# Kernel tuning notes

Measured on AMD Instinct MI355X. Metric: run time of the kernel, lower is better.

Reference implementation:

```python
import jax, jax.numpy as jnp
import numpy as np

NUM_HEADS = 8
EPS = 1e-9


def setup_inputs() -> dict:
    key = jax.random.key(0)
    ks = jax.random.split(key, 5)
    B, S, D = 2, 2048, 512
    x = jax.random.normal(ks[0], (B, S, D), dtype=jnp.float32)
    Wq = jax.random.normal(ks[1], (D, D), dtype=jnp.float32) * (1.0 / np.sqrt(D))
    Wk = jax.random.normal(ks[2], (D, D), dtype=jnp.float32) * (1.0 / np.sqrt(D))
    Wv = jax.random.normal(ks[3], (D, D), dtype=jnp.float32) * (1.0 / np.sqrt(D))
    Wo = jax.random.normal(ks[4], (D, D), dtype=jnp.float32) * (1.0 / np.sqrt(D))
    gamma = jnp.ones((D,), dtype=jnp.float32)
    beta = jnp.zeros((D,), dtype=jnp.float32)
    return {"x": x, "Wq": Wq, "Wk": Wk, "Wv": Wv, "Wo": Wo, "gamma": gamma, "beta": beta}


def _layernorm(x, gamma, beta):
    mean = jnp.mean(x, axis=-1, keepdims=True)
    var = jnp.mean(jnp.square(x - mean), axis=-1, keepdims=True)
    return gamma * ((x - mean) * jax.lax.rsqrt(var + EPS)) + beta


def reference(x, Wq, Wk, Wv, Wo, gamma, beta):
    B, S, D = x.shape
    H = NUM_HEADS
    dh = D // H
    # Note: in the original, K_V=(inputs, inputs) is captured BEFORE LayerNorm,
    # so only Q is layer-normalized; K and V use the raw inputs.
    q_in = _layernorm(x, gamma, beta)
    Q = jnp.einsum('bsd,de->bse', q_in, Wq).reshape(B, S, H, dh)
    K = jnp.einsum('bsd,de->bse', x, Wk).reshape(B, S, H, dh)
    V = jnp.einsum('bsd,de->bse', x, Wv).reshape(B, S, H, dh)
    # scaled dot-product attention (bias = 0, dropout disabled since dropout=1)
    scores = jnp.einsum('bqhd,bkhd->bhqk', Q, K) / jnp.sqrt(jnp.float32(dh))
    attn = jax.nn.softmax(scores, axis=-1)
    ctx = jnp.einsum('bhqk,bkhd->bqhd', attn, V).reshape(B, S, D)
    out = jnp.einsum('bsd,de->bse', ctx, Wo) + x  # output proj + residual
    return out
```

## Files before the change

### kernel.cpp

```cpp
#include <hip/hip_runtime.h>

typedef __bf16 bf16x8 __attribute__((ext_vector_type(8)));
typedef float f32x4 __attribute__((ext_vector_type(4)));

#define SCALE_LOG2E 0.18033688011112042f

__device__ __forceinline__ float bf2f(unsigned int u) { return __uint_as_float(u << 16); }
__device__ __forceinline__ unsigned short f2bfu(float f) {
    union { __bf16 h; unsigned short u; } v;
    v.h = (__bf16)f;
    return v.u;
}
__device__ __forceinline__ unsigned int pk2bf(float a, float b) {
    union { __bf16 h[2]; unsigned int u; } v;
    v.h[0] = (__bf16)a; v.h[1] = (__bf16)b;
    return v.u;
}

__device__ int probe_bf16(const void* xp) {
    const unsigned short* u = (const unsigned short*)xp;
    int cnt = 0;
    for (int i = 0; i < 128; i++) {
        unsigned e = (u[i] >> 7) & 0xFFu;
        cnt += (e == 0u || (e >= 0x6Cu && e <= 0x8Au)) ? 1 : 0;
    }
    return cnt >= 120;
}

__device__ __forceinline__ void load8f(const void* p, int isb, size_t idx, float* o) {
    if (isb) {
        uint4 v = *(const uint4*)((const unsigned short*)p + idx);
        o[0] = bf2f(v.x & 0xffffu); o[1] = bf2f(v.x >> 16);
        o[2] = bf2f(v.y & 0xffffu); o[3] = bf2f(v.y >> 16);
        o[4] = bf2f(v.z & 0xffffu); o[5] = bf2f(v.z >> 16);
        o[6] = bf2f(v.w & 0xffffu); o[7] = bf2f(v.w >> 16);
    } else {
        const float* f = (const float*)p + idx;
        float4 a = *(const float4*)f;
        float4 b = *(const float4*)(f + 4);
        o[0] = a.x; o[1] = a.y; o[2] = a.z; o[3] = a.w;
        o[4] = b.x; o[5] = b.y; o[6] = b.z; o[7] = b.w;
    }
}
__device__ __forceinline__ float load1f(const void* p, int isb, size_t idx) {
    return isb ? bf2f((unsigned int)((const unsigned short*)p)[idx]) : ((const float*)p)[idx];
}

__global__ __launch_bounds__(256)
void setup_k(const void* __restrict__ x, const void* __restrict__ Wq, const void* __restrict__ Wk,
             const void* __restrict__ Wv, const void* __restrict__ Wo,
             const void* __restrict__ gamma, const void* __restrict__ beta,
             unsigned short* __restrict__ xb, unsigned short* __restrict__ xn,
             unsigned short* __restrict__ WT, int* __restrict__ flags) {
    const int t = threadIdx.x;
    const int bid = blockIdx.x;
    __shared__ int shflag;
    if (bid < 1024) {
        if (t == 0) shflag = probe_bf16(Wq);
        __shared__ float tile[32][33];
        const int which = bid >> 8, tl = bid & 255;
        const int bx = (tl & 15) * 32, by = (tl >> 4) * 32;
        const void* W = (which == 0) ? Wq : (which == 1) ? Wk : (which == 2) ? Wv : Wo;
        unsigned short* dst = WT + (size_t)which * 512 * 512;
        const int xx = t & 31, y0 = t >> 5;
        __syncthreads();
        const int isb = shflag;
#pragma unroll
        for (int i = 0; i < 4; i++) {
            int y = y0 + i * 8;
            tile[y][xx] = load1f(W, isb, (size_t)(by + y) * 512 + bx + xx);
        }
        __syncthreads();
#pragma unroll
        for (int i = 0; i < 4; i++) {
            int y = y0 + i * 8;
            dst[(size_t)(bx + y) * 512 + by + xx] = f2bfu(tile[xx][y]);
        }
        return;
    }
    if (t == 0) shflag = probe_bf16(x);
    __syncthreads();
    const int isb = shflag;
    if (bid >= 1536) {
        if (t == 0) {
            flags[0] = isb;
            flags[1] = probe_bf16(Wq);
        }
        return;
    }
    const int rowbase = (bid - 1024) * 8;
    const int wv = t >> 6, lane = t & 63;
    float g[8], bb[8];
    load8f(gamma, isb, (size_t)lane * 8, g);
    load8f(beta, isb, (size_t)lane * 8, bb);
#pragma unroll
    for (int rr = 0; rr < 2; rr++) {
        const int row = rowbase + wv * 2 + rr;
        float f[8];
        load8f(x, isb, (size_t)row * 512 + lane * 8, f);
        float s = 0.f, sq = 0.f;
#pragma unroll
        for (int j = 0; j < 8; j++) { s += f[j]; sq += f[j] * f[j]; }
#pragma unroll
        for (int msk = 1; msk < 64; msk <<= 1) {
            s += __shfl_xor(s, msk);
            sq += __shfl_xor(sq, msk);
        }
        const float mean = s * (1.0f / 512.0f);
        const float var = sq * (1.0f / 512.0f) - mean * mean;
        const float rinv = rsqrtf(fmaxf(var, 0.0f) + 1e-9f);
        unsigned int pk[4];
#pragma unroll
        for (int j = 0; j < 4; j++) pk[j] = pk2bf(f[2 * j], f[2 * j + 1]);
        *(uint4*)(&xb[(size_t)row * 512 + lane * 8]) = make_uint4(pk[0], pk[1], pk[2], pk[3]);
        float ln[8];
#pragma unroll
        for (int j = 0; j < 8; j++) ln[j] = (f[j] - mean) * rinv * g[j] + bb[j];
#pragma unroll
        for (int j = 0; j < 4; j++) pk[j] = pk2bf(ln[2 * j], ln[2 * j + 1]);
        *(uint4*)(&xn[(size_t)row * 512 + lane * 8]) = make_uint4(pk[0], pk[1], pk[2], pk[3]);
    }
}

__global__ __launch_bounds__(512)
void proj_all_k(const unsigned short* __restrict__ xn, const unsigned short* __restrict__ xb,
                const unsigned short* __restrict__ WT, unsigned short* __restrict__ Qb,
                unsigned short* __restrict__ Kb, unsigned short* __restrict__ VtF) {
    __shared__ unsigned short As0[128 * 40];
    __shared__ unsigned short As1[128 * 40];
    __shared__ unsigned short Bs0[128 * 40];
    __shared__ unsigned short Bs1[128 * 40];
    const int t = threadIdx.x;
    const int w = t >> 6, lane = t & 63;
    const int quad = lane >> 4, ln = lane & 15;
    const f32x4 zero = {0.f, 0.f, 0.f, 0.f};
    const int rA = t >> 2, cA = t & 3;
    const int soff = rA * 40 + cA * 8;

    if (blockIdx.z == 0) {
        const int role = blockIdx.x & 1;
        const int n0 = (blockIdx.x >> 1) * 128;
        const int m0 = blockIdx.y * 128;
        const unsigned short* Axp = role ? xb : xn;
        const unsigned short* BT = WT + (size_t)role * 512 * 512;
        unsigned short* out = role ? Kb : Qb;
        const int wm = w & 1, wn = w >> 1;

        f32x4 acc[4][2];
#pragma unroll
        for (int i = 0; i < 4; i++)
#pragma unroll
            for (int j = 0; j < 2; j++) acc[i][j] = zero;

        const unsigned short* const gA = Axp + (size_t)(m0 + rA) * 512 + cA * 8;
        const unsigned short* const gB = BT + (size_t)(n0 + rA) * 512 + cA * 8;
        uint4 pa = *(const uint4*)(gA);
        uint4 pb = *(const uint4*)(gB);

#define PROJ_CMP(AS, BS)                                                          \
        {                                                                         \
            bf16x8 af[4], bfr[2];                                                 \
            _Pragma("unroll")                                                     \
            for (int i = 0; i < 4; i++)                                           \
                af[i] = *(const bf16x8*)(&AS[(wm * 64 + i * 16 + ln) * 40 + quad * 8]); \
            _Pragma("unroll")                                                     \
            for (int j = 0; j < 2; j++)                                           \
                bfr[j] = *(const bf16x8*)(&BS[(wn * 32 + j * 16 + ln) * 40 + quad * 8]); \
            _Pragma("unroll")                                                     \
            for (int i = 0; i < 4; i++)                                           \
                _Pragma("unroll")                                                 \
                for (int j = 0; j < 2; j++)                                       \
                    acc[i][j] = __builtin_amdgcn_mfma_f32_16x16x32_bf16(af[i], bfr[j], acc[i][j], 0, 0, 0); \
        }

        for (int kt = 0; kt < 512; kt += 64) {
            *(uint4*)(&As0[soff]) = pa;
            *(uint4*)(&Bs0[soff]) = pb;
            __syncthreads();
            pa = *(const uint4*)(gA + kt + 32);
            pb = *(const uint4*)(gB + kt + 32);
            PROJ_CMP(As0, Bs0);
            *(uint4*)(&As1[soff]) = pa;
            *(uint4*)(&Bs1[soff]) = pb;
            __syncthreads();
            if (kt + 64 < 512) {
                pa = *(const uint4*)(gA + kt + 64);
                pb = *(const uint4*)(gB + kt + 64);
            }
            PROJ_CMP(As1, Bs1);
        }
#undef PROJ_CMP
#pragma unroll
        for (int i = 0; i < 4; i++)
#pragma unroll
            for (int j = 0; j < 2; j++)
#pragma unroll
                for (int r = 0; r < 4; r++) {
                    int grow = m0 + wm * 64 + i * 16 + quad * 4 + r;
                    int gcol = n0 + wn * 32 + j * 16 + ln;
                    float v = acc[i][j][r];
                    if (role == 0) v *= SCALE_LOG2E;
                    out[(size_t)grow * 512 + gcol] = f2bfu(v);
                }
    } else {
        const int m0 = blockIdx.x * 64;
        const int n0 = blockIdx.y * 128;
        const unsigned short* AW = WT + (size_t)2 * 512 * 512;
        const int wv = w & 3, wn2 = w >> 2;

        f32x4 acc[4];
#pragma unroll
        for (int j = 0; j < 4; j++) acc[j] = zero;

        const unsigned short* const gA = AW + (size_t)(m0 + rA) * 512 + cA * 8;
        const unsigned short* const gB = xb + (size_t)(n0 + rA) * 512 + cA * 8;
        uint4 pa, pb;
        if (t < 256) pa = *(const uint4*)(gA);
        pb = *(const uint4*)(gB);

#define PROJV_CMP(AS, BS)                                                         \
        {                                                                         \
            bf16x8 af = *(const bf16x8*)(&AS[(wv * 16 + ln) * 40 + quad * 8]);    \
            _Pragma("unroll")                                                     \
            for (int j = 0; j < 4; j++) {                                         \
                bf16x8 bfr = *(const bf16x8*)(&BS[(wn2 * 64 + j * 16 + ln) * 40 + quad * 8]); \
                acc[j] = __builtin_amdgcn_mfma_f32_16x16x32_bf16(af, bfr, acc[j], 0, 0, 0); \
            }                                                                     \
        }

        for (int kt = 0; kt < 512; kt += 64) {
            if (t < 256) *(uint4*)(&As0[soff]) = pa;
            *(uint4*)(&Bs0[soff]) = pb;
            __syncthreads();
            if (t < 256) pa = *(const uint4*)(gA + kt + 32);
            pb = *(const uint4*)(gB + kt + 32);
            PROJV_CMP(As0, Bs0);
            if (t < 256) *(uint4*)(&As1[soff]) = pa;
            *(uint4*)(&Bs1[soff]) = pb;
            __syncthreads();
            if (kt + 64 < 512) {
                if (t < 256) pa = *(const uint4*)(gA + kt + 64);
                pb = *(const uint4*)(gB + kt + 64);
            }
            PROJV_CMP(As1, Bs1);
        }
#undef PROJV_CMP
#pragma unroll
        for (int j = 0; j < 4; j++)
#pragma unroll
            for (int r = 0; r < 4; r++) {
                int grow = m0 + wv * 16 + quad * 4 + r;
                int gcol = n0 + wn2 * 64 + j * 16 + ln;
                VtF[(size_t)grow * 4096 + gcol] = f2bfu(acc[j][r]);
            }
    }
}

__global__ __launch_bounds__(1024, 1)
void attn_m_k(const unsigned short* __restrict__ Qb, const unsigned short* __restrict__ Kb,
              const unsigned short* __restrict__ VtF, unsigned short* __restrict__ ctx) {
    const int S = 2048, PT = 72, NT = 32;
    const int t = threadIdx.x;
    const int bid = blockIdx.x;
    const int lid = (bid & 7) * 32 + (bid >> 3);
    const int qb = lid & 15, h = (lid >> 4) & 7, b = lid >> 7;
    const int w = t >> 6, lane = t & 63;
    const int quad = lane >> 4, ln = lane & 15;
    const int kq = w & 3, qh = w >> 2;

    __shared__ unsigned short sh[27648];
    unsigned short* const KsA = sh;
    unsigned short* const KsB = sh + 4608;
    unsigned short* const Vt0 = sh + 9216;
    unsigned short* const Vt1 = sh + 13824;
    unsigned short* const Vt2 = sh + 18432;
    unsigned short* const Vt3 = sh + 23040;
    unsigned short* const Qs  = sh + 18432;

    const size_t baseQ  = (size_t)(b * S + qb * 128) * 512 + h * 64;
    const size_t baseK  = (size_t)(b * S) * 512 + h * 64;
    const size_t baseVt = (size_t)(h * 64) * 4096 + (size_t)b * S;

    const int c8 = t & 7;
    const int r64 = (t & 511) >> 3;
    const int stoff = r64 * PT + c8 * 8;

    const int kfo0 = (kq * 16 + ln) * PT + quad * 8;
    const int vto  = ln * PT + kq * 16 + quad * 4;

    const unsigned short* const gK = Kb + baseK + (size_t)r64 * 512 + c8 * 8;
    const unsigned short* const gV = VtF + baseVt + (size_t)r64 * 4096 + c8 * 8;

    uint4 sa, sb;
    if (t < 512) { sa = *(const uint4*)(gK); sb = *(const uint4*)(gK + 32768); }
    else         { sa = *(const uint4*)(gV); sb = *(const uint4*)(gV + 64); }

    {
        const int rQ = t >> 3;
        *(uint4*)(&Qs[rQ * PT + c8 * 8]) = *(const uint4*)(Qb + baseQ + (size_t)rQ * 512 + c8 * 8);
    }
    __syncthreads();
    bf16x8 qf[2][2];
#pragma unroll
    for (int s2 = 0; s2 < 2; s2++)
#pragma unroll
        for (int i = 0; i < 2; i++)
            qf[s2][i] = *(const bf16x8*)(&Qs[(qh * 32 + s2 * 16 + ln) * PT + quad * 8 + 32 * i]);

    f32x4 acc[2][4];
    const f32x4 zero = {0.f, 0.f, 0.f, 0.f};
#pragma unroll
    for (int s2 = 0; s2 < 2; s2++)
#pragma unroll
        for (int j = 0; j < 4; j++) acc[s2][j] = zero;
    float lsum0 = 0.f, lsum1 = 0.f;

#define STAGE(KS, VT, R)                                                    \
    {                                                                       \
        if (t < 512) *(uint4*)(&KS[stoff]) = R;                             \
        else         *(uint4*)(&VT[stoff]) = R;                             \
    }
#define PRELOAD(R, kt)                                                      \
    if ((kt) < NT) {                                                        \
        if (t < 512) R = *(const uint4*)(gK + (size_t)(kt) * 32768);        \
        else         R = *(const uint4*)(gV + (size_t)(kt) * 64);           \
    }
#define QK_EXP(KS, U00, U01, U10, U11)                                      \
    {                                                                       \
        bf16x8 kf0 = *(const bf16x8*)(&KS[kfo0]);                           \
        bf16x8 kf1 = *(const bf16x8*)(&KS[kfo0 + 32]);                      \
        f32x4 sc0 = zero, sc1 = zero;                                       \
        sc0 = __builtin_amdgcn_mfma_f32_16x16x32_bf16(kf0, qf[0][0], sc0, 0, 0, 0); \
        sc0 = __builtin_amdgcn_mfma_f32_16x16x32_bf16(kf1, qf[0][1], sc0, 0, 0, 0); \
        sc1 = __builtin_amdgcn_mfma_f32_16x16x32_bf16(kf0, qf[1][0], sc1, 0, 0, 0); \
        sc1 = __builtin_amdgcn_mfma_f32_16x16x32_bf16(kf1, qf[1][1], sc1, 0, 0, 0); \
        float a0 = __builtin_amdgcn_exp2f(fminf(sc0[0], 30.f));             \
        float a1 = __builtin_amdgcn_exp2f(fminf(sc0[1], 30.f));             \
        float a2 = __builtin_amdgcn_exp2f(fminf(sc0[2], 30.f));             \
        float a3 = __builtin_amdgcn_exp2f(fminf(sc0[3], 30.f));             \
        lsum0 += (a0 + a1) + (a2 + a3);                                     \
        U00 = pk2bf(a0, a1); U01 = pk2bf(a2, a3);                           \
        float b0 = __builtin_amdgcn_exp2f(fminf(sc1[0], 30.f));             \
        float b1 = __builtin_amdgcn_exp2f(fminf(sc1[1], 30.f));             \
        float b2 = __builtin_amdgcn_exp2f(fminf(sc1[2], 30.f));             \
        float b3 = __builtin_amdgcn_exp2f(fminf(sc1[3], 30.f));             \
        lsum1 += (b0 + b1) + (b2 + b3);                                     \
        U10 = pk2bf(b0, b1); U11 = pk2bf(b2, b3);                           \
    }
#define PV4(VTE, VTO)                                                       \
    {                                                                       \
        bf16x8 ap0 = __builtin_bit_cast(bf16x8, make_uint4(uA00, uA01, uB00, uB01)); \
        bf16x8 ap1 = __builtin_bit_cast(bf16x8, make_uint4(uA10, uA11, uB10, uB11)); \
        _Pragma("unroll")                                                   \
        for (int nt = 0; nt < 4; nt++) {                                    \
            uint2 ve = *(const uint2*)(&VTE[vto + nt * 16 * PT]);           \
            uint2 vo = *(const uint2*)(&VTO[vto + nt * 16 * PT]);           \
            bf16x8 vb = __builtin_bit_cast(bf16x8, make_uint4(ve.x, ve.y, vo.x, vo.y)); \
            acc[0][nt] = __builtin_amdgcn_mfma_f32_16x16x32_bf16(ap0, vb, acc[0][nt], 0, 0, 0); \
            acc[1][nt] = __builtin_amdgcn_mfma_f32_16x16x32_bf16(ap1, vb, acc[1][nt], 0, 0, 0); \
        }                                                                   \
    }

    for (int m = 0; m < 8; m++) {
        const int T = m * 4;
        unsigned int uA00, uA01, uA10, uA11, uB00, uB01, uB10, uB11;
        STAGE(KsA, Vt0, sa);
        __syncthreads();
        PRELOAD(sa, T + 2);
        QK_EXP(KsA, uA00, uA01, uA10, uA11);
        STAGE(KsB, Vt1, sb);
        __syncthreads();
        PRELOAD(sb, T + 3);
        QK_EXP(KsB, uB00, uB01, uB10, uB11);
        PV4(Vt0, Vt1);
        STAGE(KsA, Vt2, sa);
        __syncthreads();
        PRELOAD(sa, T + 4);
        QK_EXP(KsA, uA00, uA01, uA10, uA11);
        STAGE(KsB, Vt3, sb);
        __syncthreads();
        PRELOAD(sb, T + 5);
        QK_EXP(KsB, uB00, uB01, uB10, uB11);
        PV4(Vt2, Vt3);
    }
#undef STAGE
#undef PRELOAD
#undef QK_EXP
#undef PV4

    lsum0 += __shfl_xor(lsum0, 16);
    lsum0 += __shfl_xor(lsum0, 32);
    lsum1 += __shfl_xor(lsum1, 16);
    lsum1 += __shfl_xor(lsum1, 32);

    __syncthreads();
    float* scr  = (float*)sh;
    float* lred = scr + 13056;
    if (quad == 0) {
        lred[kq * 128 + qh * 32 + ln] = lsum0;
        lred[kq * 128 + qh * 32 + 16 + ln] = lsum1;
    }
#pragma unroll
    for (int rr = 0; rr < 2; rr++) {
        __syncthreads();
        if ((qh >> 1) == rr && kq != 0) {
            const int pb = (kq - 1) * 4352 + ((qh & 1) * 32 + quad * 4) * 68 + ln;
#pragma unroll
            for (int s2 = 0; s2 < 2; s2++)
#pragma unroll
                for (int nt = 0; nt < 4; nt++)
#pragma unroll
                    for (int r = 0; r < 4; r++)
                        scr[pb + (s2 * 16 + r) * 68 + nt * 16] = acc[s2][nt][r];
        }
        __syncthreads();
        if ((qh >> 1) == rr && kq == 0) {
#pragma unroll
            for (int s2 = 0; s2 < 2; s2++) {
                const size_t baseO = (size_t)(b * S + qb * 128 + qh * 32 + s2 * 16 + quad * 4) * 512 + h * 64 + ln;
#pragma unroll
                for (int r = 0; r < 4; r++) {
                    int qrow = qh * 32 + s2 * 16 + quad * 4 + r;
                    float lt = lred[qrow] + lred[128 + qrow] + lred[256 + qrow] + lred[384 + qrow];
                    float inv = 1.0f / lt;
                    int rb = ((qh & 1) * 32 + s2 * 16 + quad * 4 + r) * 68 + ln;
#pragma unroll
                    for (int nt = 0; nt < 4; nt++) {
                        float v = acc[s2][nt][r] + scr[rb + nt * 16] + scr[4352 + rb + nt * 16] + scr[8704 + rb + nt * 16];
                        ctx[baseO + (size_t)r * 512 + nt * 16] = f2bfu(v * inv);
                    }
                }
            }
        }
    }
}

__global__ __launch_bounds__(512)
void outproj_k(const unsigned short* __restrict__ ctx, const unsigned short* __restrict__ BT,
               const void* __restrict__ x, void* __restrict__ outp, const int* __restrict__ flags) {
    __shared__ unsigned short As0[64 * 40];
    __shared__ unsigned short As1[64 * 40];
    __shared__ unsigned short Bs0[64 * 40];
    __shared__ unsigned short Bs1[64 * 40];
    const int t = threadIdx.x;
    const int isb = flags[0];
    const int m0 = blockIdx.y * 64, n0 = blockIdx.x * 64;
    const int w = t >> 6, lane = t & 63;
    const int wm = w & 3, wn = w >> 2;
    const int quad = lane >> 4, ln = lane & 15;

    const int rs = (t & 255) >> 2, cs = t & 3;
    const int soff = rs * 40 + cs * 8;
    const int isA = t < 256;
    const unsigned short* gsrc = isA ? (ctx + (size_t)(m0 + rs) * 512 + cs * 8)
                                     : (BT + (size_t)(n0 + rs) * 512 + cs * 8);

    f32x4 acc[2];
    const f32x4 zero = {0.f, 0.f, 0.f, 0.f};
    acc[0] = zero; acc[1] = zero;

    uint4 ps = *(const uint4*)(gsrc);

#define OUTP_CMP(AS, BS)                                                          \
    {                                                                             \
        bf16x8 af = *(const bf16x8*)(&AS[(wm * 16 + ln) * 40 + quad * 8]);        \
        _Pragma("unroll")                                                         \
        for (int j = 0; j < 2; j++) {                                             \
            bf16x8 bfr = *(const bf16x8*)(&BS[(wn * 32 + j * 16 + ln) * 40 + quad * 8]); \
            acc[j] = __builtin_amdgcn_mfma_f32_16x16x32_bf16(af, bfr, acc[j], 0, 0, 0); \
        }                                                                         \
    }

    for (int kt = 0; kt < 512; kt += 64) {
        if (isA) *(uint4*)(&As0[soff]) = ps;
        else     *(uint4*)(&Bs0[soff]) = ps;
        __syncthreads();
        ps = *(const uint4*)(gsrc + kt + 32);
        OUTP_CMP(As0, Bs0);
        if (isA) *(uint4*)(&As1[soff]) = ps;
        else     *(uint4*)(&Bs1[soff]) = ps;
        __syncthreads();
        if (kt + 64 < 512) ps = *(const uint4*)(gsrc + kt + 64);
        OUTP_CMP(As1, Bs1);
    }
#undef OUTP_CMP
#pragma unroll
    for (int j = 0; j < 2; j++)
#pragma unroll
        for (int r = 0; r < 4; r++) {
            int grow = m0 + wm * 16 + quad * 4 + r;
            int gcol = n0 + wn * 32 + j * 16 + ln;
            size_t idx = (size_t)grow * 512 + gcol;
            float v = acc[j][r] + load1f(x, isb, idx);
            if (isb) ((unsigned short*)outp)[idx] = f2bfu(v);
            else     ((float*)outp)[idx] = v;
        }
}

__global__ __launch_bounds__(256)
void fill_k(unsigned short* out, int n) {
    int i = blockIdx.x * 256 + threadIdx.x;
    if (i < n) out[i] = 0x4442;
}

extern "C" void kernel_launch(void* const* d_in, const int* in_sizes, int n_in,
                              void* d_out, int out_size, void* d_ws, size_t ws_size,
                              hipStream_t stream) {
    const void* x     = d_in[0];
    const void* Wq    = d_in[1];
    const void* Wk    = d_in[2];
    const void* Wv    = d_in[3];
    const void* Wo    = d_in[4];
    const void* gamma = d_in[5];
    const void* beta  = d_in[6];

    const size_t NW = 512 * 512;
    const size_t NX = 4096 * 512;
    char* w = (char*)d_ws;

    const size_t XB_OFF = 2097152 + 3 * NX * 2;
    const size_t XN_OFF = XB_OFF + NX * 2;
    const size_t FLAGS_OFF = XN_OFF + NX * 2;
    const size_t NEED_FULL = FLAGS_OFF + 16;

    if (ws_size < NEED_FULL) {
        fill_k<<<(out_size + 255) / 256, 256, 0, stream>>>((unsigned short*)d_out, out_size);
        return;
    }

    unsigned short* WT  = (unsigned short*)w;
    unsigned short* Qb  = (unsigned short*)(w + 2097152);
    unsigned short* Kb  = Qb + NX;
    unsigned short* VtF = Kb + NX;
    unsigned short* ctx = Qb;
    unsigned short* xb  = (unsigned short*)(w + XB_OFF);
    unsigned short* xn  = (unsigned short*)(w + XN_OFF);
    int* flags = (int*)(w + FLAGS_OFF);

    setup_k<<<1537, 256, 0, stream>>>(x, Wq, Wk, Wv, Wo, gamma, beta, xb, xn, WT, flags);
    proj_all_k<<<dim3(8, 32, 2), 512, 0, stream>>>(xn, xb, WT, Qb, Kb, VtF);
    attn_m_k<<<256, 1024, 0, stream>>>(Qb, Kb, VtF, ctx);
    outproj_k<<<dim3(8, 64), 512, 0, stream>>>(ctx, WT + 3 * NW, x, d_out, flags);
}
```

Before: 141.1 us.

## Stage 128-key tiles with triple-buffered LDS in attention to halve barriers

The attention main loop now stages 128 keys per step instead of 64, loading two K rows and two Vt chunks per thread, and rotates through three LDS buffers in place of the old two-K/four-V scheme. Each step does one barrier and covers both 64-key halves (QK for both, then PV), so the number of __syncthreads per block drops from 32 to 16. LDS use roughly doubles to about 108KB. With one 1024-thread block per CU this should still fit, but it leaves less room and spends more registers on prefetching two tiles at once.

```diff
diff --git a/kernel.cpp b/kernel.cpp
--- a/kernel.cpp
+++ b/kernel.cpp
@@ -162,10 +162,10 @@
             bf16x8 af[4], bfr[2];                                                 \
             _Pragma("unroll")                                                     \
             for (int i = 0; i < 4; i++)                                           \
-                af[i] = *(const bf16x8*)(&AS[(wm * 64 + i * 16 + ln) * 40 + quad * 8]); \
+                af[i] = *(const bf16x8*)(&(AS)[(wm * 64 + i * 16 + ln) * 40 + quad * 8]); \
             _Pragma("unroll")                                                     \
             for (int j = 0; j < 2; j++)                                           \
-                bfr[j] = *(const bf16x8*)(&BS[(wn * 32 + j * 16 + ln) * 40 + quad * 8]); \
+                bfr[j] = *(const bf16x8*)(&(BS)[(wn * 32 + j * 16 + ln) * 40 + quad * 8]); \
             _Pragma("unroll")                                                     \
             for (int i = 0; i < 4; i++)                                           \
                 _Pragma("unroll")                                                 \
@@ -220,10 +220,10 @@
 
 #define PROJV_CMP(AS, BS)                                                         \
         {                                                                         \
-            bf16x8 af = *(const bf16x8*)(&AS[(wv * 16 + ln) * 40 + quad * 8]);    \
+            bf16x8 af = *(const bf16x8*)(&(AS)[(wv * 16 + ln) * 40 + quad * 8]);  \
             _Pragma("unroll")                                                     \
             for (int j = 0; j < 4; j++) {                                         \
-                bf16x8 bfr = *(const bf16x8*)(&BS[(wn2 * 64 + j * 16 + ln) * 40 + quad * 8]); \
+                bf16x8 bfr = *(const bf16x8*)(&(BS)[(wn2 * 64 + j * 16 + ln) * 40 + quad * 8]); \
                 acc[j] = __builtin_amdgcn_mfma_f32_16x16x32_bf16(af, bfr, acc[j], 0, 0, 0); \
             }                                                                     \
         }
@@ -259,7 +259,7 @@
 __global__ __launch_bounds__(1024, 1)
 void attn_m_k(const unsigned short* __restrict__ Qb, const unsigned short* __restrict__ Kb,
               const unsigned short* __restrict__ VtF, unsigned short* __restrict__ ctx) {
-    const int S = 2048, PT = 72, NT = 32;
+    const int S = 2048, PT = 72;
     const int t = threadIdx.x;
     const int bid = blockIdx.x;
     const int lid = (bid & 7) * 32 + (bid >> 3);
@@ -268,32 +268,43 @@
     const int quad = lane >> 4, ln = lane & 15;
     const int kq = w & 3, qh = w >> 2;
 
-    __shared__ unsigned short sh[27648];
-    unsigned short* const KsA = sh;
-    unsigned short* const KsB = sh + 4608;
-    unsigned short* const Vt0 = sh + 9216;
-    unsigned short* const Vt1 = sh + 13824;
-    unsigned short* const Vt2 = sh + 18432;
-    unsigned short* const Vt3 = sh + 23040;
-    unsigned short* const Qs  = sh + 18432;
+    __shared__ unsigned short sh[55296];
+    unsigned short* const Ks0 = sh;
+    unsigned short* const Ks1 = sh + 9216;
+    unsigned short* const Ks2 = sh + 18432;
+    unsigned short* const Vt0 = sh + 27648;
+    unsigned short* const Vt1 = sh + 36864;
+    unsigned short* const Vt2 = sh + 46080;
+    unsigned short* const Qs  = sh + 46080;
 
     const size_t baseQ  = (size_t)(b * S + qb * 128) * 512 + h * 64;
     const size_t baseK  = (size_t)(b * S) * 512 + h * 64;
     const size_t baseVt = (size_t)(h * 64) * 4096 + (size_t)b * S;
 
     const int c8 = t & 7;
-    const int r64 = (t & 511) >> 3;
-    const int stoff = r64 * PT + c8 * 8;
+    const int isK = t < 512;
+    const int o0 = t & 511;
+
+    const int kr0 = o0 >> 3;
+    const int stK0 = kr0 * PT + c8 * 8;
+    const int stK1 = stK0 + 64 * PT;
+    const unsigned short* const gK0 = Kb + baseK + (size_t)kr0 * 512 + c8 * 8;
+    const unsigned short* const gK1 = gK0 + (size_t)64 * 512;
+
+    const int vd0 = o0 >> 4, vc0 = o0 & 15;
+    const int o1v = o0 + 512;
+    const int vd1 = o1v >> 4, vc1 = o1v & 15;
+    const int stV0 = vd0 * PT + (vc0 & 7) * 8 + (vc0 >> 3) * 4608;
+    const int stV1 = vd1 * PT + (vc1 & 7) * 8 + (vc1 >> 3) * 4608;
+    const unsigned short* const gV0 = VtF + baseVt + (size_t)vd0 * 4096 + vc0 * 8;
+    const unsigned short* const gV1 = VtF + baseVt + (size_t)vd1 * 4096 + vc1 * 8;
 
     const int kfo0 = (kq * 16 + ln) * PT + quad * 8;
     const int vto  = ln * PT + kq * 16 + quad * 4;
 
-    const unsigned short* const gK = Kb + baseK + (size_t)r64 * 512 + c8 * 8;
-    const unsigned short* const gV = VtF + baseVt + (size_t)r64 * 4096 + c8 * 8;
-
-    uint4 sa, sb;
-    if (t < 512) { sa = *(const uint4*)(gK); sb = *(const uint4*)(gK + 32768); }
-    else         { sa = *(const uint4*)(gV); sb = *(const uint4*)(gV + 64); }
+    uint4 pr0, pr1;
+    if (isK) { pr0 = *(const uint4*)(gK0); pr1 = *(const uint4*)(gK1); }
+    else     { pr0 = *(const uint4*)(gV0); pr1 = *(const uint4*)(gV1); }
 
     {
         const int rQ = t >> 3;
@@ -315,20 +326,22 @@
         for (int j = 0; j < 4; j++) acc[s2][j] = zero;
     float lsum0 = 0.f, lsum1 = 0.f;
 
-#define STAGE(KS, VT, R)                                                    \
+#define STAGE(KS, VT)                                                       \
     {                                                                       \
-        if (t < 512) *(uint4*)(&KS[stoff]) = R;                             \
-        else         *(uint4*)(&VT[stoff]) = R;                             \
-    }
-#define PRELOAD(R, kt)                                                      \
-    if ((kt) < NT) {                                                        \
-        if (t < 512) R = *(const uint4*)(gK + (size_t)(kt) * 32768);        \
-        else         R = *(const uint4*)(gV + (size_t)(kt) * 64);           \
-    }
-#define QK_EXP(KS, U00, U01, U10, U11)                                      \
+        if (isK) { *(uint4*)(&(KS)[stK0]) = pr0; *(uint4*)(&(KS)[stK1]) = pr1; } \
+        else     { *(uint4*)(&(VT)[stV0]) = pr0; *(uint4*)(&(VT)[stV1]) = pr1; } \
+    }
+#define PRELOAD(T)                                                          \
+    if ((T) < 16) {                                                         \
+        if (isK) { pr0 = *(const uint4*)(gK0 + (size_t)(T) * 65536);        \
+                   pr1 = *(const uint4*)(gK1 + (size_t)(T) * 65536); }      \
+        else     { pr0 = *(const uint4*)(gV0 + (T) * 128);                  \
+                   pr1 = *(const uint4*)(gV1 + (T) * 128); }                \
+    }
+#define QK_EXP(KS, HOFF, U00, U01, U10, U11)                                \
     {                                                                       \
-        bf16x8 kf0 = *(const bf16x8*)(&KS[kfo0]);                           \
-        bf16x8 kf1 = *(const bf16x8*)(&KS[kfo0 + 32]);                      \
+        bf16x8 kf0 = *(const bf16x8*)(&(KS)[kfo0 + (HOFF)]);                \
+        bf16x8 kf1 = *(const bf16x8*)(&(KS)[kfo0 + (HOFF) + 32]);           \
         f32x4 sc0 = zero, sc1 = zero;                                       \
         sc0 = __builtin_amdgcn_mfma_f32_16x16x32_bf16(kf0, qf[0][0], sc0, 0, 0, 0); \
         sc0 = __builtin_amdgcn_mfma_f32_16x16x32_bf16(kf1, qf[0][1], sc0, 0, 0, 0); \
@@ -353,40 +366,36 @@
         bf16x8 ap1 = __builtin_bit_cast(bf16x8, make_uint4(uA10, uA11, uB10, uB11)); \
         _Pragma("unroll")                                                   \
         for (int nt = 0; nt < 4; nt++) {                                    \
-            uint2 ve = *(const uint2*)(&VTE[vto + nt * 16 * PT]);           \
-            uint2 vo = *(const uint2*)(&VTO[vto + nt * 16 * PT]);           \
+            uint2 ve = *(const uint2*)(&(VTE)[vto + nt * 16 * PT]);         \
+            uint2 vo = *(const uint2*)(&(VTO)[vto + nt * 16 * PT]);         \
             bf16x8 vb = __builtin_bit_cast(bf16x8, make_uint4(ve.x, ve.y, vo.x, vo.y)); \
             acc[0][nt] = __builtin_amdgcn_mfma_f32_16x16x32_bf16(ap0, vb, acc[0][nt], 0, 0, 0); \
             acc[1][nt] = __builtin_amdgcn_mfma_f32_16x16x32_bf16(ap1, vb, acc[1][nt], 0, 0, 0); \
         }                                                                   \
     }
-
-    for (int m = 0; m < 8; m++) {
-        const int T = m * 4;
-        unsigned int uA00, uA01, uA10, uA11, uB00, uB01, uB10, uB11;
-        STAGE(KsA, Vt0, sa);
-        __syncthreads();
-        PRELOAD(sa, T + 2);
-        QK_EXP(KsA, uA00, uA01, uA10, uA11);
-        STAGE(KsB, Vt1, sb);
-        __syncthreads();
-        PRELOAD(sb, T + 3);
-        QK_EXP(KsB, uB00, uB01, uB10, uB11);
-        PV4(Vt0, Vt1);
-        STAGE(KsA, Vt2, sa);
-        __syncthreads();
-        PRELOAD(sa, T + 4);
-        QK_EXP(KsA, uA00, uA01, uA10, uA11);
-        STAGE(KsB, Vt3, sb);
-        __syncthreads();
-        PRELOAD(sb, T + 5);
-        QK_EXP(KsB, uB00, uB01, uB10, uB11);
-        PV4(Vt2, Vt3);
-    }
+#define ATTN_ITER(KS, VT, T)                                                \
+    {                                                                       \
+        unsigned int uA00, uA01, uA10, uA11, uB00, uB01, uB10, uB11;        \
+        STAGE(KS, VT);                                                      \
+        __syncthreads();                                                    \
+        PRELOAD((T) + 1);                                                   \
+        QK_EXP(KS, 0, uA00, uA01, uA10, uA11);                              \
+        QK_EXP(KS, 64 * PT, uB00, uB01, uB10, uB11);                        \
+        PV4(VT, (VT) + 4608);                                               \
+    }
+
+    for (int m = 0; m < 5; m++) {
+        const int T = m * 3;
+        ATTN_ITER(Ks0, Vt0, T);
+        ATTN_ITER(Ks1, Vt1, T + 1);
+        ATTN_ITER(Ks2, Vt2, T + 2);
+    }
+    ATTN_ITER(Ks0, Vt0, 15);
 #undef STAGE
 #undef PRELOAD
 #undef QK_EXP
 #undef PV4
+#undef ATTN_ITER
 
     lsum0 += __shfl_xor(lsum0, 16);
     lsum0 += __shfl_xor(lsum0, 32);
@@ -463,10 +472,10 @@
 
 #define OUTP_CMP(AS, BS)                                                          \
     {                                                                             \
-        bf16x8 af = *(const bf16x8*)(&AS[(wm * 16 + ln) * 40 + quad * 8]);        \
+        bf16x8 af = *(const bf16x8*)(&(AS)[(wm * 16 + ln) * 40 + quad * 8]);      \
         _Pragma("unroll")                                                         \
         for (int j = 0; j < 2; j++) {                                             \
-            bf16x8 bfr = *(const bf16x8*)(&BS[(wn * 32 + j * 16 + ln) * 40 + quad * 8]); \
+            bf16x8 bfr = *(const bf16x8*)(&(BS)[(wn * 32 + j * 16 + ln) * 40 + quad * 8]); \
             acc[j] = __builtin_amdgcn_mfma_f32_16x16x32_bf16(af, bfr, acc[j], 0, 0, 0); \
         }                                                                         \
     }
```

Result: no change. 139.8 us (-0.9%).
